# Optimization experiments

Hardware: AMD Instinct MI355X
Metric: run time of the kernel (lower is better)

Reference implementation:

```python
import jax, jax.numpy as jnp
import numpy as np

N_NODES = 100000
N_EDGES = 400000
D_IN = 128
D_OUT = 128
BN_EPS = 1e-5


def setup_inputs() -> dict:
    key = jax.random.key(0)
    k1, k2, k3, k4, k5 = jax.random.split(key, 5)
    n_feat = jax.random.normal(k1, (N_NODES, D_IN), dtype=jnp.float32)
    edge_index = jax.random.randint(k2, (2, N_EDGES), 0, N_NODES, dtype=jnp.int32)
    edge_weight = jnp.ones((N_EDGES,), dtype=jnp.float32)
    # learned params: BatchNorm1d affine + Linear(in, out, bias=False)
    gamma = jnp.ones((D_IN,), dtype=jnp.float32) + 0.1 * jax.random.normal(k3, (D_IN,), dtype=jnp.float32)
    beta = 0.1 * jax.random.normal(k4, (D_IN,), dtype=jnp.float32)
    W = jax.random.normal(k5, (D_OUT, D_IN), dtype=jnp.float32) * (1.0 / np.sqrt(D_IN))
    return {"n_feat": n_feat, "edge_index": edge_index, "edge_weight": edge_weight,
            "gamma": gamma, "beta": beta, "W": W}


def reference(n_feat, edge_index, edge_weight, gamma, beta, W):
    # BatchNorm1d (training-mode batch stats, biased variance) -> ReLU -> Linear (no bias)
    mu = jnp.mean(n_feat, axis=0)
    var = jnp.mean(jnp.square(n_feat - mu), axis=0)
    xh = (n_feat - mu) * jax.lax.rsqrt(var + BN_EPS)
    y = jax.nn.relu(gamma * xh + beta)
    h = y @ W.T  # [N, D_OUT]
    # sparse adjacency matmul: out[row] += w * h[col]
    row, col = edge_index[0], edge_index[1]
    msgs = h[col] * edge_weight[:, None]          # gather, [E, D_OUT]
    agg = jax.ops.segment_sum(msgs, row, num_segments=N_NODES)
    return h * h + agg
```

## Files before the change

### kernel.cpp

```cpp
#include <hip/hip_runtime.h>

#define N_NODES 100000
#define N_EDGES 400000
#define D 128
#define BN_EPS 1e-5f
#define ELL_CAP 32

#define NSTAT 64
#define CS_BLOCKS 625
#define CS_ITER 20
#define FILL_BLOCKS 1563
#define GEMM_BLOCKS 782

#define WS_STATS   0
#define WS_DEG2    (NSTAT * 256)
#define WS_HB      (WS_DEG2 + N_NODES)
#define WS_ELL2    (WS_HB + N_NODES * D / 2)
#define WS_ELL2_END (WS_ELL2 + N_NODES * ELL_CAP * 2)
#define WS_WB      WS_ELL2_END
#define WS_ELL_END2 (WS_WB + 8192)
#define WS_SCALE   (NSTAT * 256)
#define WS_SHIFT   (WS_SCALE + 128)
#define WS_WT      (WS_SHIFT + 128)
#define WS_H       (WS_WT + D * D)
#define WS_DEG     (WS_H + N_NODES * D)
#define WS_ROWPTR  (WS_DEG + N_NODES)
#define WS_CURSOR  (WS_ROWPTR + N_NODES + 1)
#define WS_CSRCOL  (WS_CURSOR + N_NODES)
#define WS_CSRW    (WS_CSRCOL + N_EDGES)
#define WS_END     (WS_CSRW + N_EDGES)

typedef __attribute__((ext_vector_type(8))) short short8;
typedef __attribute__((ext_vector_type(4))) float f32x4;

static __device__ __forceinline__ unsigned short f2bf(float f) {
    union { float f; unsigned u; } v; v.f = f;
    unsigned r = v.u + 0x7FFF + ((v.u >> 16) & 1);
    return (unsigned short)(r >> 16);
}
static __device__ __forceinline__ float bf2f(unsigned short b) {
    union { unsigned u; float f; } v; v.u = ((unsigned)b) << 16;
    return v.f;
}
static __device__ __forceinline__ unsigned short f2h(float f) {
    union { _Float16 h; unsigned short u; } v; v.h = (_Float16)f;
    return v.u;
}
static __device__ __forceinline__ float h2f(unsigned short u) {
    union { unsigned short u; _Float16 h; } v; v.u = u;
    return (float)v.h;
}

__global__ __launch_bounds__(256) void fused_pre_kernel(const float* __restrict__ x,
                                                        float* __restrict__ stats,
                                                        const int* __restrict__ ei,
                                                        const float* __restrict__ ew,
                                                        int* __restrict__ deg,
                                                        int2* __restrict__ ell2,
                                                        const float* __restrict__ W,
                                                        unsigned short* __restrict__ Wb) {
    int b = blockIdx.x;
    int t = threadIdx.x;
    if (b < CS_BLOCKS) {
        int tid = b * 256 + t;
        const int NTH = CS_BLOCKS * 256;
        const float4* x4 = (const float4*)x;
        float4 v[CS_ITER];
        #pragma unroll
        for (int i = 0; i < CS_ITER; i++) v[i] = x4[tid + i * NTH];
        __builtin_amdgcn_sched_barrier(0);
        float4 s = {0.f, 0.f, 0.f, 0.f};
        float4 q = {0.f, 0.f, 0.f, 0.f};
        #pragma unroll
        for (int i = 0; i < CS_ITER; i++) {
            s.x += v[i].x; s.y += v[i].y; s.z += v[i].z; s.w += v[i].w;
            q.x += v[i].x * v[i].x; q.y += v[i].y * v[i].y;
            q.z += v[i].z * v[i].z; q.w += v[i].w * v[i].w;
        }
        __shared__ float4 ss[256];
        __shared__ float4 sq[256];
        ss[t] = s;
        sq[t] = q;
        __syncthreads();
        if (t < 32) {
            float4 a = ss[t];
            float4 bb = sq[t];
            for (int i = 32; i < 256; i += 32) {
                float4 t1 = ss[t + i];
                float4 t2 = sq[t + i];
                a.x += t1.x; a.y += t1.y; a.z += t1.z; a.w += t1.w;
                bb.x += t2.x; bb.y += t2.y; bb.z += t2.z; bb.w += t2.w;
            }
            float* st = stats + (b % NSTAT) * 256;
            int colb = (t * 4) & 127;
            atomicAdd(&st[colb + 0], a.x);
            atomicAdd(&st[colb + 1], a.y);
            atomicAdd(&st[colb + 2], a.z);
            atomicAdd(&st[colb + 3], a.w);
            atomicAdd(&st[128 + colb + 0], bb.x);
            atomicAdd(&st[128 + colb + 1], bb.y);
            atomicAdd(&st[128 + colb + 2], bb.z);
            atomicAdd(&st[128 + colb + 3], bb.w);
        }
    } else if (b < CS_BLOCKS + FILL_BLOCKS) {
        int e = (b - CS_BLOCKS) * 256 + t;
        if (e >= N_EDGES) return;
        int r = ei[e];
        int c = ei[N_EDGES + e];
        float w = ew[e];
        int slot = atomicAdd(&deg[r], 1);
        if (slot < ELL_CAP) ell2[r * ELL_CAP + slot] = make_int2(c, __float_as_int(w));
    } else {
        int i = (b - CS_BLOCKS - FILL_BLOCKS) * 256 + t;
        float4 v = *(const float4*)(W + i * 4);
        ushort4 o;
        o.x = f2bf(v.x); o.y = f2bf(v.y); o.z = f2bf(v.z); o.w = f2bf(v.w);
        *(ushort4*)(Wb + i * 4) = o;
    }
}

#define YPAD 136
__global__ __launch_bounds__(256, 4) void gemm_mfma8_kernel(const float* __restrict__ x,
                                                            const float* __restrict__ stats,
                                                            const float* __restrict__ gamma,
                                                            const float* __restrict__ beta,
                                                            const unsigned short* __restrict__ Wb,
                                                            unsigned short* __restrict__ hh) {
    __shared__ __align__(16) unsigned short Yl[64 * YPAD];
    __shared__ float sscale[128];
    __shared__ float sshift[128];
    int t = threadIdx.x;
    int lane = t & 63;
    int wave = t >> 6;
    int m16  = lane & 15;
    int quad = lane >> 4;
    int wrow0 = wave * 16;
    int c4 = (t & 31) * 4;

    if (t < 128) {
        float sum = 0.f, sq = 0.f;
        #pragma unroll 16
        for (int c = 0; c < NSTAT; c++) {
            sum += stats[c * 256 + t];
            sq  += stats[c * 256 + 128 + t];
        }
        float mu  = sum * (1.0f / N_NODES);
        float var = sq * (1.0f / N_NODES) - mu * mu;
        float sc  = gamma[t] * rsqrtf(var + BN_EPS);
        sscale[t] = sc;
        sshift[t] = beta[t] - mu * sc;
    }
    __syncthreads();
    float4 sc = *(const float4*)(sscale + c4);
    float4 sh = *(const float4*)(sshift + c4);

    const unsigned short* wb = Wb + m16 * D + quad * 8;
    const unsigned short* yl = Yl + (wrow0 + m16) * YPAD + quad * 8;

    #pragma unroll
    for (int half = 0; half < 2; half++) {
        int row0 = (blockIdx.x * 2 + half) * 64;

        float4 xv[8];
        #pragma unroll
        for (int p = 0; p < 8; p++) {
            int r = (t + p * 256) >> 5;
            int grow = row0 + r;
            int srow = grow < N_NODES ? grow : N_NODES - 1;
            xv[p] = *(const float4*)(x + (size_t)srow * D + c4);
        }
        #pragma unroll
        for (int p = 0; p < 8; p++) {
            int r = (t + p * 256) >> 5;
            ushort4 y;
            y.x = f2bf(fmaxf(fmaf(xv[p].x, sc.x, sh.x), 0.f));
            y.y = f2bf(fmaxf(fmaf(xv[p].y, sc.y, sh.y), 0.f));
            y.z = f2bf(fmaxf(fmaf(xv[p].z, sc.z, sh.z), 0.f));
            y.w = f2bf(fmaxf(fmaf(xv[p].w, sc.w, sh.w), 0.f));
            *(ushort4*)(Yl + r * YPAD + c4) = y;
        }
        __syncthreads();

        f32x4 acc[8];
        #pragma unroll
        for (int nt = 0; nt < 8; nt++) acc[nt] = (f32x4){0.f, 0.f, 0.f, 0.f};

        #pragma unroll
        for (int kc = 0; kc < 4; kc++) {
            short8 a = *(const short8*)(yl + kc * 32);
            #pragma unroll
            for (int nt = 0; nt < 8; nt++) {
                short8 b = *(const short8*)(wb + nt * 16 * D + kc * 32);
                acc[nt] = __builtin_amdgcn_mfma_f32_16x16x32_bf16(a, b, acc[nt], 0, 0, 0);
            }
        }

        #pragma unroll
        for (int r = 0; r < 4; r++) {
            int grow = row0 + wrow0 + quad * 4 + r;
            if (grow < N_NODES) {
                unsigned short* hrow = hh + (size_t)grow * D + m16;
                #pragma unroll
                for (int nt = 0; nt < 8; nt++) {
                    hrow[nt * 16] = f2h(acc[nt][r]);
                }
            }
        }
        __syncthreads();
    }
}

__global__ __launch_bounds__(256) void gather_ell7_kernel(const int* __restrict__ deg,
                                                          const int2* __restrict__ ell2,
                                                          const unsigned short* __restrict__ hh,
                                                          float* __restrict__ out) {
    int lane = threadIdx.x & 15;
    int n = blockIdx.x * 16 + (threadIdx.x >> 4);
    if (n >= N_NODES) return;
    short8 hself = *(const short8*)(hh + (size_t)n * D + lane * 8);
    int dg = __builtin_nontemporal_load(&deg[n]);
    if (dg > ELL_CAP) dg = ELL_CAP;
    int dg16 = dg < 16 ? dg : 16;

    int2 my = make_int2(0, 0);
    if (lane < dg16) my = ell2[n * ELL_CAP + lane];

    float acc[8] = {0.f, 0.f, 0.f, 0.f, 0.f, 0.f, 0.f, 0.f};
    int s = 0;
    for (; s + 4 <= dg16; s += 4) {
        int   c0 = __shfl(my.x, s + 0, 16); float w0 = __int_as_float(__shfl(my.y, s + 0, 16));
        int   c1 = __shfl(my.x, s + 1, 16); float w1 = __int_as_float(__shfl(my.y, s + 1, 16));
        int   c2 = __shfl(my.x, s + 2, 16); float w2 = __int_as_float(__shfl(my.y, s + 2, 16));
        int   c3 = __shfl(my.x, s + 3, 16); float w3 = __int_as_float(__shfl(my.y, s + 3, 16));
        short8 v0 = *(const short8*)(hh + (size_t)c0 * D + lane * 8);
        short8 v1 = *(const short8*)(hh + (size_t)c1 * D + lane * 8);
        short8 v2 = *(const short8*)(hh + (size_t)c2 * D + lane * 8);
        short8 v3 = *(const short8*)(hh + (size_t)c3 * D + lane * 8);
        #pragma unroll
        for (int j = 0; j < 8; j++) {
            acc[j] = fmaf(w0, h2f((unsigned short)v0[j]), acc[j]);
            acc[j] = fmaf(w1, h2f((unsigned short)v1[j]), acc[j]);
            acc[j] = fmaf(w2, h2f((unsigned short)v2[j]), acc[j]);
            acc[j] = fmaf(w3, h2f((unsigned short)v3[j]), acc[j]);
        }
    }
    for (; s < dg16; s++) {
        int c = __shfl(my.x, s, 16);
        float w = __int_as_float(__shfl(my.y, s, 16));
        short8 v = *(const short8*)(hh + (size_t)c * D + lane * 8);
        #pragma unroll
        for (int j = 0; j < 8; j++) acc[j] = fmaf(w, h2f((unsigned short)v[j]), acc[j]);
    }
    for (s = 16; s < dg; s++) {
        int2 cw = ell2[n * ELL_CAP + s];
        float w = __int_as_float(cw.y);
        short8 v = *(const short8*)(hh + (size_t)cw.x * D + lane * 8);
        #pragma unroll
        for (int j = 0; j < 8; j++) acc[j] = fmaf(w, h2f((unsigned short)v[j]), acc[j]);
    }

    f32x4 a, b;
    {
        float h0 = h2f((unsigned short)hself[0]); float h1 = h2f((unsigned short)hself[1]);
        float h2 = h2f((unsigned short)hself[2]); float h3 = h2f((unsigned short)hself[3]);
        float h4 = h2f((unsigned short)hself[4]); float h5 = h2f((unsigned short)hself[5]);
        float h6 = h2f((unsigned short)hself[6]); float h7 = h2f((unsigned short)hself[7]);
        a[0] = fmaf(h0, h0, acc[0]); a[1] = fmaf(h1, h1, acc[1]);
        a[2] = fmaf(h2, h2, acc[2]); a[3] = fmaf(h3, h3, acc[3]);
        b[0] = fmaf(h4, h4, acc[4]); b[1] = fmaf(h5, h5, acc[5]);
        b[2] = fmaf(h6, h6, acc[6]); b[3] = fmaf(h7, h7, acc[7]);
    }
    float* o = out + (size_t)n * D + lane * 8;
    __builtin_nontemporal_store(a, (f32x4*)o);
    __builtin_nontemporal_store(b, (f32x4*)(o + 4));
}

__global__ __launch_bounds__(256) void colstats_kernel(const float* __restrict__ x,
                                                       float* __restrict__ stats,
                                                       int* __restrict__ deg) {
    int tid = blockIdx.x * 256 + threadIdx.x;
    if (deg && tid < N_NODES) deg[tid] = 0;
    const int NTH = CS_BLOCKS * 256;
    const float4* x4 = (const float4*)x;
    float4 v[CS_ITER];
    #pragma unroll
    for (int i = 0; i < CS_ITER; i++) v[i] = x4[tid + i * NTH];
    __builtin_amdgcn_sched_barrier(0);
    float4 s = {0.f, 0.f, 0.f, 0.f};
    float4 q = {0.f, 0.f, 0.f, 0.f};
    #pragma unroll
    for (int i = 0; i < CS_ITER; i++) {
        s.x += v[i].x; s.y += v[i].y; s.z += v[i].z; s.w += v[i].w;
        q.x += v[i].x * v[i].x; q.y += v[i].y * v[i].y;
        q.z += v[i].z * v[i].z; q.w += v[i].w * v[i].w;
    }
    __shared__ float4 ss[256];
    __shared__ float4 sq[256];
    ss[threadIdx.x] = s;
    sq[threadIdx.x] = q;
    __syncthreads();
    if (threadIdx.x < 32) {
        float4 a = ss[threadIdx.x];
        float4 b = sq[threadIdx.x];
        for (int i = 32; i < 256; i += 32) {
            float4 t1 = ss[threadIdx.x + i];
            float4 t2 = sq[threadIdx.x + i];
            a.x += t1.x; a.y += t1.y; a.z += t1.z; a.w += t1.w;
            b.x += t2.x; b.y += t2.y; b.z += t2.z; b.w += t2.w;
        }
        float* st = stats + (blockIdx.x % NSTAT) * 256;
        int colb = (threadIdx.x * 4) & 127;
        atomicAdd(&st[colb + 0], a.x);
        atomicAdd(&st[colb + 1], a.y);
        atomicAdd(&st[colb + 2], a.z);
        atomicAdd(&st[colb + 3], a.w);
        atomicAdd(&st[128 + colb + 0], b.x);
        atomicAdd(&st[128 + colb + 1], b.y);
        atomicAdd(&st[128 + colb + 2], b.z);
        atomicAdd(&st[128 + colb + 3], b.w);
    }
}

__global__ __launch_bounds__(128) void finalize_kernel(const float* __restrict__ stats,
                                                       const float* __restrict__ gamma,
                                                       const float* __restrict__ beta,
                                                       float* __restrict__ scale,
                                                       float* __restrict__ shift) {
    int d = threadIdx.x;
    float sum = 0.f, sq = 0.f;
    #pragma unroll 16
    for (int c = 0; c < NSTAT; c++) {
        sum += stats[c * 256 + d];
        sq  += stats[c * 256 + 128 + d];
    }
    float mu  = sum * (1.0f / N_NODES);
    float var = sq * (1.0f / N_NODES) - mu * mu;
    float sc  = gamma[d] * rsqrtf(var + BN_EPS);
    scale[d] = sc;
    shift[d] = beta[d] - mu * sc;
}

__global__ __launch_bounds__(256) void transposeW_kernel(const float* __restrict__ W,
                                                         float* __restrict__ Wt) {
    int i = blockIdx.x * blockDim.x + threadIdx.x;
    if (i < D * D) {
        int j = i >> 7;
        int k = i & 127;
        Wt[k * D + j] = W[i];
    }
}

template <int WRITE_SQ>
__global__ __launch_bounds__(256) void gemm_kernel(const float* __restrict__ x,
                                                   const float* __restrict__ scale,
                                                   const float* __restrict__ shift,
                                                   const float* __restrict__ Wt,
                                                   float* __restrict__ h,
                                                   float* __restrict__ out) {
    __shared__ float Ws[D * D];
    __shared__ float Ys[32 * D];
    int t = threadIdx.x;
    const float4* Wt4 = (const float4*)Wt;
    float4* Ws4 = (float4*)Ws;
    #pragma unroll 4
    for (int i = t; i < D * D / 4; i += 256) Ws4[i] = Wt4[i];
    int row0 = blockIdx.x * 32;
    const float4* x4 = (const float4*)(x + (size_t)row0 * D);
    float4* Ys4 = (float4*)Ys;
    #pragma unroll 2
    for (int i = t; i < 32 * D / 4; i += 256) {
        int c4 = (i & 31) * 4;
        float4 v = x4[i];
        v.x = fmaxf(fmaf(v.x, scale[c4 + 0], shift[c4 + 0]), 0.f);
        v.y = fmaxf(fmaf(v.y, scale[c4 + 1], shift[c4 + 1]), 0.f);
        v.z = fmaxf(fmaf(v.z, scale[c4 + 2], shift[c4 + 2]), 0.f);
        v.w = fmaxf(fmaf(v.w, scale[c4 + 3], shift[c4 + 3]), 0.f);
        Ys4[i] = v;
    }
    __syncthreads();
    int cg2 = t & 31;
    int rg = t >> 5;
    float4 acc[4] = {{0,0,0,0},{0,0,0,0},{0,0,0,0},{0,0,0,0}};
    #pragma unroll 2
    for (int k = 0; k < D; k += 4) {
        float4 w0 = *(const float4*)&Ws[(k + 0) * D + cg2 * 4];
        float4 w1 = *(const float4*)&Ws[(k + 1) * D + cg2 * 4];
        float4 w2 = *(const float4*)&Ws[(k + 2) * D + cg2 * 4];
        float4 w3 = *(const float4*)&Ws[(k + 3) * D + cg2 * 4];
        #pragma unroll
        for (int r = 0; r < 4; r++) {
            float4 y = *(const float4*)&Ys[(rg * 4 + r) * D + k];
            acc[r].x = fmaf(y.x, w0.x, fmaf(y.y, w1.x, fmaf(y.z, w2.x, fmaf(y.w, w3.x, acc[r].x))));
            acc[r].y = fmaf(y.x, w0.y, fmaf(y.y, w1.y, fmaf(y.z, w2.y, fmaf(y.w, w3.y, acc[r].y))));
            acc[r].z = fmaf(y.x, w0.z, fmaf(y.y, w1.z, fmaf(y.z, w2.z, fmaf(y.w, w3.z, acc[r].z))));
            acc[r].w = fmaf(y.x, w0.w, fmaf(y.y, w1.w, fmaf(y.z, w2.w, fmaf(y.w, w3.w, acc[r].w))));
        }
    }
    #pragma unroll
    for (int r = 0; r < 4; r++) {
        size_t row = (size_t)row0 + rg * 4 + r;
        float4 v = acc[r];
        *(float4*)&h[row * D + cg2 * 4] = v;
        if (WRITE_SQ) {
            float4 sqv = {v.x * v.x, v.y * v.y, v.z * v.z, v.w * v.w};
            *(float4*)&out[row * D + cg2 * 4] = sqv;
        }
    }
}

__global__ __launch_bounds__(256) void hist_kernel(const int* __restrict__ ei,
                                                   int* __restrict__ deg) {
    int e = blockIdx.x * 256 + threadIdx.x;
    if (e < N_EDGES) atomicAdd(&deg[ei[e]], 1);
}

__global__ __launch_bounds__(1024) void scan_kernel(const int* __restrict__ deg,
                                                    int* __restrict__ row_ptr,
                                                    int* __restrict__ cursor) {
    __shared__ int part[1024];
    int t = threadIdx.x;
    const int CHUNK = 100;
    int base = t * CHUNK;
    int s = 0;
    if (base < N_NODES) {
        for (int i = 0; i < CHUNK; i++) s += deg[base + i];
    }
    part[t] = s;
    __syncthreads();
    for (int off = 1; off < 1024; off <<= 1) {
        int v = (t >= off) ? part[t - off] : 0;
        __syncthreads();
        part[t] += v;
        __syncthreads();
    }
    int pre = (t == 0) ? 0 : part[t - 1];
    if (base < N_NODES) {
        for (int i = 0; i < CHUNK; i++) {
            row_ptr[base + i] = pre;
            cursor[base + i] = pre;
            pre += deg[base + i];
        }
    }
    if (t == 1023) row_ptr[N_NODES] = part[1023];
}

__global__ __launch_bounds__(256) void fill_kernel(const int* __restrict__ ei,
                                                   const float* __restrict__ ew,
                                                   int* __restrict__ cursor,
                                                   int* __restrict__ csr_col,
                                                   float* __restrict__ csr_w) {
    int e = blockIdx.x * 256 + threadIdx.x;
    if (e >= N_EDGES) return;
    int r = ei[e];
    int c = ei[N_EDGES + e];
    int slot = atomicAdd(&cursor[r], 1);
    csr_col[slot] = c;
    csr_w[slot] = ew[e];
}

__global__ __launch_bounds__(256) void gather_kernel(const int* __restrict__ row_ptr,
                                                     const int* __restrict__ csr_col,
                                                     const float* __restrict__ csr_w,
                                                     const float* __restrict__ h,
                                                     float* __restrict__ out) {
    int lane = threadIdx.x & 31;
    int n = blockIdx.x * 8 + (threadIdx.x >> 5);
    if (n >= N_NODES) return;
    int s0 = row_ptr[n];
    int s1 = row_ptr[n + 1];
    float4 acc = {0.f, 0.f, 0.f, 0.f};
    for (int s = s0; s < s1; s++) {
        int c = csr_col[s];
        float w = csr_w[s];
        float4 v = *(const float4*)&h[(size_t)c * D + lane * 4];
        acc.x = fmaf(w, v.x, acc.x);
        acc.y = fmaf(w, v.y, acc.y);
        acc.z = fmaf(w, v.z, acc.z);
        acc.w = fmaf(w, v.w, acc.w);
    }
    float4 hv = *(const float4*)&h[(size_t)n * D + lane * 4];
    float4 o;
    o.x = fmaf(hv.x, hv.x, acc.x);
    o.y = fmaf(hv.y, hv.y, acc.y);
    o.z = fmaf(hv.z, hv.z, acc.z);
    o.w = fmaf(hv.w, hv.w, acc.w);
    *(float4*)&out[(size_t)n * D + lane * 4] = o;
}

__global__ __launch_bounds__(256) void scatter_kernel(const int* __restrict__ ei,
                                                      const float* __restrict__ ew,
                                                      const float* __restrict__ h,
                                                      float* __restrict__ out) {
    int lane = threadIdx.x & 31;
    int e = blockIdx.x * 8 + (threadIdx.x >> 5);
    if (e >= N_EDGES) return;
    int r = ei[e];
    int c = ei[N_EDGES + e];
    float w = ew[e];
    float4 v = *(const float4*)&h[(size_t)c * D + lane * 4];
    float* o = out + (size_t)r * D + lane * 4;
    atomicAdd(o + 0, v.x * w);
    atomicAdd(o + 1, v.y * w);
    atomicAdd(o + 2, v.z * w);
    atomicAdd(o + 3, v.w * w);
}

extern "C" void kernel_launch(void* const* d_in, const int* in_sizes, int n_in,
                              void* d_out, int out_size, void* d_ws, size_t ws_size,
                              hipStream_t stream) {
    const float* n_feat = (const float*)d_in[0];
    const int*   ei     = (const int*)d_in[1];
    const float* ew     = (const float*)d_in[2];
    const float* gamma  = (const float*)d_in[3];
    const float* beta   = (const float*)d_in[4];
    const float* W      = (const float*)d_in[5];
    float* out = (float*)d_out;

    float* ws    = (float*)d_ws;
    float* stats = ws + WS_STATS;

    bool ell_ok = ws_size >= (size_t)WS_ELL_END2 * sizeof(float);
    bool csr_ok = ws_size >= (size_t)WS_END * sizeof(float);

    if (ell_ok) {
        unsigned short* hh  = (unsigned short*)(ws + WS_HB);
        int*  deg  = (int*)ws + WS_DEG2;
        int2* ell2 = (int2*)((int*)ws + WS_ELL2);
        unsigned short* Wb = (unsigned short*)(ws + WS_WB);

        (void)hipMemsetAsync(stats, 0, (NSTAT * 256 + N_NODES) * sizeof(float), stream);
        fused_pre_kernel<<<CS_BLOCKS + FILL_BLOCKS + 16, 256, 0, stream>>>(
            n_feat, stats, ei, ew, deg, ell2, W, Wb);
        gemm_mfma8_kernel<<<GEMM_BLOCKS, 256, 0, stream>>>(n_feat, stats, gamma, beta, Wb, hh);
        gather_ell7_kernel<<<(N_NODES + 15) / 16, 256, 0, stream>>>(deg, ell2, hh, out);
    } else if (csr_ok) {
        float* scale = ws + WS_SCALE;
        float* shift = ws + WS_SHIFT;
        float* Wt    = ws + WS_WT;
        float* h     = ws + WS_H;
        int*   deg     = (int*)ws + WS_DEG;
        int*   row_ptr = (int*)ws + WS_ROWPTR;
        int*   cursor  = (int*)ws + WS_CURSOR;
        int*   csr_col = (int*)ws + WS_CSRCOL;
        float* csr_w   = ws + WS_CSRW;

        (void)hipMemsetAsync(stats, 0, NSTAT * 256 * sizeof(float), stream);
        colstats_kernel<<<CS_BLOCKS, 256, 0, stream>>>(n_feat, stats, nullptr);
        finalize_kernel<<<1, 128, 0, stream>>>(stats, gamma, beta, scale, shift);
        transposeW_kernel<<<64, 256, 0, stream>>>(W, Wt);
        (void)hipMemsetAsync(deg, 0, N_NODES * sizeof(int), stream);
        gemm_kernel<0><<<N_NODES / 32, 256, 0, stream>>>(n_feat, scale, shift, Wt, h, out);
        hist_kernel<<<(N_EDGES + 255) / 256, 256, 0, stream>>>(ei, deg);
        scan_kernel<<<1, 1024, 0, stream>>>(deg, row_ptr, cursor);
        fill_kernel<<<(N_EDGES + 255) / 256, 256, 0, stream>>>(ei, ew, cursor, csr_col, csr_w);
        gather_kernel<<<(N_NODES + 7) / 8, 256, 0, stream>>>(row_ptr, csr_col, csr_w, h, out);
    } else {
        float* scale = ws + WS_SCALE;
        float* shift = ws + WS_SHIFT;
        float* Wt    = ws + WS_WT;
        float* h     = ws + WS_H;
        (void)hipMemsetAsync(stats, 0, NSTAT * 256 * sizeof(float), stream);
        colstats_kernel<<<CS_BLOCKS, 256, 0, stream>>>(n_feat, stats, nullptr);
        finalize_kernel<<<1, 128, 0, stream>>>(stats, gamma, beta, scale, shift);
        transposeW_kernel<<<64, 256, 0, stream>>>(W, Wt);
        gemm_kernel<1><<<N_NODES / 32, 256, 0, stream>>>(n_feat, scale, shift, Wt, h, out);
        scatter_kernel<<<(N_EDGES + 7) / 8, 256, 0, stream>>>(ei, ew, h, out);
    }
}
```

Before: 193.1 us.

## Load GEMM A-operand directly into MFMA registers, dropping LDS staging

The BN+ReLU+linear GEMM kernel now has each lane load its own 16x32 A-fragment of x straight from global memory into registers. It applies scale/shift/ReLU and the bf16 conversion in registers, so the LDS tile, its writes and its barriers are gone. Each block now handles one 64-row tile instead of two, which doubles the grid. The x loads are issued before the stats reduction and kept there by a sched_barrier, so load latency can overlap the finalize work. The trade-off is that global loads are less coalesced (32-byte segments per lane) and the per-block stats finalize is repeated across twice as many blocks.

```diff
diff --git a/kernel.cpp b/kernel.cpp
--- a/kernel.cpp
+++ b/kernel.cpp
@@ -10,7 +10,6 @@
 #define CS_BLOCKS 625
 #define CS_ITER 20
 #define FILL_BLOCKS 1563
-#define GEMM_BLOCKS 782
 
 #define WS_STATS   0
 #define WS_DEG2    (NSTAT * 256)
@@ -119,14 +118,12 @@
     }
 }
 
-#define YPAD 136
-__global__ __launch_bounds__(256, 4) void gemm_mfma8_kernel(const float* __restrict__ x,
+__global__ __launch_bounds__(256, 4) void gemm_mfma9_kernel(const float* __restrict__ x,
                                                             const float* __restrict__ stats,
                                                             const float* __restrict__ gamma,
                                                             const float* __restrict__ beta,
                                                             const unsigned short* __restrict__ Wb,
                                                             unsigned short* __restrict__ hh) {
-    __shared__ __align__(16) unsigned short Yl[64 * YPAD];
     __shared__ float sscale[128];
     __shared__ float sshift[128];
     int t = threadIdx.x;
@@ -134,8 +131,18 @@
     int wave = t >> 6;
     int m16  = lane & 15;
     int quad = lane >> 4;
-    int wrow0 = wave * 16;
-    int c4 = (t & 31) * 4;
+    int row0 = blockIdx.x * 64;
+
+    int arow = row0 + wave * 16 + m16;
+    int srow = arow < N_NODES ? arow : N_NODES - 1;
+    const float* xr = x + (size_t)srow * D + quad * 8;
+    float4 xa[4][2];
+    #pragma unroll
+    for (int kc = 0; kc < 4; kc++) {
+        xa[kc][0] = *(const float4*)(xr + kc * 32);
+        xa[kc][1] = *(const float4*)(xr + kc * 32 + 4);
+    }
+    __builtin_amdgcn_sched_barrier(0);
 
     if (t < 128) {
         float sum = 0.f, sq = 0.f;
@@ -151,62 +158,44 @@
         sshift[t] = beta[t] - mu * sc;
     }
     __syncthreads();
-    float4 sc = *(const float4*)(sscale + c4);
-    float4 sh = *(const float4*)(sshift + c4);
+
+    f32x4 acc[8];
+    #pragma unroll
+    for (int nt = 0; nt < 8; nt++) acc[nt] = (f32x4){0.f, 0.f, 0.f, 0.f};
 
     const unsigned short* wb = Wb + m16 * D + quad * 8;
-    const unsigned short* yl = Yl + (wrow0 + m16) * YPAD + quad * 8;
-
-    #pragma unroll
-    for (int half = 0; half < 2; half++) {
-        int row0 = (blockIdx.x * 2 + half) * 64;
-
-        float4 xv[8];
-        #pragma unroll
-        for (int p = 0; p < 8; p++) {
-            int r = (t + p * 256) >> 5;
-            int grow = row0 + r;
-            int srow = grow < N_NODES ? grow : N_NODES - 1;
-            xv[p] = *(const float4*)(x + (size_t)srow * D + c4);
-        }
-        #pragma unroll
-        for (int p = 0; p < 8; p++) {
-            int r = (t + p * 256) >> 5;
-            ushort4 y;
-            y.x = f2bf(fmaxf(fmaf(xv[p].x, sc.x, sh.x), 0.f));
-            y.y = f2bf(fmaxf(fmaf(xv[p].y, sc.y, sh.y), 0.f));
-            y.z = f2bf(fmaxf(fmaf(xv[p].z, sc.z, sh.z), 0.f));
-            y.w = f2bf(fmaxf(fmaf(xv[p].w, sc.w, sh.w), 0.f));
-            *(ushort4*)(Yl + r * YPAD + c4) = y;
-        }
-        __syncthreads();
-
-        f32x4 acc[8];
-        #pragma unroll
-        for (int nt = 0; nt < 8; nt++) acc[nt] = (f32x4){0.f, 0.f, 0.f, 0.f};
-
-        #pragma unroll
-        for (int kc = 0; kc < 4; kc++) {
-            short8 a = *(const short8*)(yl + kc * 32);
+    #pragma unroll
+    for (int kc = 0; kc < 4; kc++) {
+        float4 s0 = *(const float4*)(sscale + kc * 32 + quad * 8);
+        float4 s1 = *(const float4*)(sscale + kc * 32 + quad * 8 + 4);
+        float4 h0 = *(const float4*)(sshift + kc * 32 + quad * 8);
+        float4 h1 = *(const float4*)(sshift + kc * 32 + quad * 8 + 4);
+        short8 a;
+        a[0] = (short)f2bf(fmaxf(fmaf(xa[kc][0].x, s0.x, h0.x), 0.f));
+        a[1] = (short)f2bf(fmaxf(fmaf(xa[kc][0].y, s0.y, h0.y), 0.f));
+        a[2] = (short)f2bf(fmaxf(fmaf(xa[kc][0].z, s0.z, h0.z), 0.f));
+        a[3] = (short)f2bf(fmaxf(fmaf(xa[kc][0].w, s0.w, h0.w), 0.f));
+        a[4] = (short)f2bf(fmaxf(fmaf(xa[kc][1].x, s1.x, h1.x), 0.f));
+        a[5] = (short)f2bf(fmaxf(fmaf(xa[kc][1].y, s1.y, h1.y), 0.f));
+        a[6] = (short)f2bf(fmaxf(fmaf(xa[kc][1].z, s1.z, h1.z), 0.f));
+        a[7] = (short)f2bf(fmaxf(fmaf(xa[kc][1].w, s1.w, h1.w), 0.f));
+        #pragma unroll
+        for (int nt = 0; nt < 8; nt++) {
+            short8 b = *(const short8*)(wb + nt * 16 * D + kc * 32);
+            acc[nt] = __builtin_amdgcn_mfma_f32_16x16x32_bf16(a, b, acc[nt], 0, 0, 0);
+        }
+    }
+
+    #pragma unroll
+    for (int r = 0; r < 4; r++) {
+        int grow = row0 + wave * 16 + quad * 4 + r;
+        if (grow < N_NODES) {
+            unsigned short* hrow = hh + (size_t)grow * D + m16;
             #pragma unroll
             for (int nt = 0; nt < 8; nt++) {
-                short8 b = *(const short8*)(wb + nt * 16 * D + kc * 32);
-                acc[nt] = __builtin_amdgcn_mfma_f32_16x16x32_bf16(a, b, acc[nt], 0, 0, 0);
+                hrow[nt * 16] = f2h(acc[nt][r]);
             }
         }
-
-        #pragma unroll
-        for (int r = 0; r < 4; r++) {
-            int grow = row0 + wrow0 + quad * 4 + r;
-            if (grow < N_NODES) {
-                unsigned short* hrow = hh + (size_t)grow * D + m16;
-                #pragma unroll
-                for (int nt = 0; nt < 8; nt++) {
-                    hrow[nt * 16] = f2h(acc[nt][r]);
-                }
-            }
-        }
-        __syncthreads();
     }
 }
 
@@ -531,7 +520,7 @@
         (void)hipMemsetAsync(stats, 0, (NSTAT * 256 + N_NODES) * sizeof(float), stream);
         fused_pre_kernel<<<CS_BLOCKS + FILL_BLOCKS + 16, 256, 0, stream>>>(
             n_feat, stats, ei, ew, deg, ell2, W, Wb);
-        gemm_mfma8_kernel<<<GEMM_BLOCKS, 256, 0, stream>>>(n_feat, stats, gamma, beta, Wb, hh);
+        gemm_mfma9_kernel<<<(N_NODES + 63) / 64, 256, 0, stream>>>(n_feat, stats, gamma, beta, Wb, hh);
         gather_ell7_kernel<<<(N_NODES + 15) / 16, 256, 0, stream>>>(deg, ell2, hh, out);
     } else if (csr_ok) {
         float* scale = ws + WS_SCALE;
```

Result: no change. 194.7 us (+0.8%).
